# Performance work log

Measured on AMD Instinct MI355X. Metric: run time of the kernel, lower is better.

Reference implementation:

```python
import jax, jax.numpy as jnp
import numpy as np

B, LQ, LA, H = 32, 1024, 1024, 512
NEG_INF = jnp.float32(-1e7)  # matches torch masked_fill_(-10000000.0)


def setup_inputs() -> dict:
    key = jax.random.key(0)
    k1, k2, k3, k4 = jax.random.split(key, 4)
    q = jax.random.normal(k1, (B, LQ, H), dtype=jnp.float32)
    a = jax.random.normal(k2, (B, LA, H), dtype=jnp.float32)
    q_mask = jax.random.randint(k3, (B, LQ, 1), 0, 2).astype(jnp.int32)
    a_mask = jax.random.randint(k4, (B, LA, 1), 0, 2).astype(jnp.int32)
    # learned scalar, initialized exactly as in __init__
    temperature = jnp.float32(1.0 / np.sqrt(H))
    return {"q": q, "a": a, "q_mask": q_mask, "a_mask": a_mask,
            "temperature": temperature}


def reference(q, a, q_mask, a_mask, temperature):
    # scaled co-attention scores: [B, Lq, La]
    attn = jnp.einsum('bqh,bah->bqa', q, a) * temperature
    # validity mask via outer product of per-token masks (nonzero = valid)
    mask = jnp.matmul(q_mask.astype(jnp.float32),
                      a_mask.transpose(0, 2, 1).astype(jnp.float32)) != 0
    attn = jnp.where(mask, attn, NEG_INF)
    # dual-axis softmax over the SAME score matrix
    attn_q = jax.nn.softmax(attn, axis=1)  # normalize over Lq
    attn_a = jax.nn.softmax(attn, axis=2)  # normalize over La
    # aggregation: a_s = attn_q^T @ q -> [B, La, H]; q_s = attn_a @ a -> [B, Lq, H]
    a_s = jnp.einsum('bqa,bqh->bah', attn_q, q)
    q_s = jnp.einsum('bqa,bah->bqh', attn_a, a)
    return (jnp.concatenate([q, q_s], axis=-1),
            jnp.concatenate([a, a_s], axis=-1))
```

## Files before the change

### kernel.cpp

```cpp
#include <hip/hip_runtime.h>
#include <cstdint>
#include <cstddef>

#define NB   32
#define LQA  1024
#define HD   512

typedef __attribute__((ext_vector_type(4))) float  f32x4;
typedef __attribute__((ext_vector_type(8))) short  s16x8;
typedef __attribute__((ext_vector_type(4))) unsigned short u16x4;

static __device__ __forceinline__ unsigned short f2bf(float f) {
  unsigned int u = __builtin_bit_cast(unsigned int, f);
  u += 0x7fffu + ((u >> 16) & 1u);
  return (unsigned short)(u >> 16);
}
static __device__ __forceinline__ float bf2f(unsigned short h) {
  unsigned int u = ((unsigned int)h) << 16;
  return __builtin_bit_cast(float, u);
}
static __device__ __forceinline__ u16x4 cvt4(f32x4 v) {
  u16x4 r;
  r.x = f2bf(v.x); r.y = f2bf(v.y); r.z = f2bf(v.z); r.w = f2bf(v.w);
  return r;
}

typedef __attribute__((address_space(1))) const void gas_void;
typedef __attribute__((address_space(3))) void las_void;
static __device__ __forceinline__ void gload_lds16(const void* g, void* l) {
  __builtin_amdgcn_global_load_lds((gas_void*)g, (las_void*)l, 16, 0, 0);
}

__global__ __launch_bounds__(256) void k_prep(
    const float* __restrict__ qsrc, const float* __restrict__ asrc,
    float* __restrict__ out0, float* __restrict__ out1,
    unsigned short* __restrict__ qT, unsigned short* __restrict__ aT,
    unsigned short* __restrict__ qb16, unsigned short* __restrict__ ab16,
    float* __restrict__ qsum, float* __restrict__ asum)
{
  const int bz  = blockIdx.z;
  const int isA = bz >> 5;
  const int b   = bz & 31;
  const int h0 = blockIdx.x * 64;
  const int q0 = blockIdx.y * 64;
  const int t  = threadIdx.x;

  const float* src = isA ? asrc : qsrc;
  float* out_left      = isA ? out1 : out0;
  unsigned short* dstT = isA ? aT : qT;
  unsigned short* dstN = isA ? ab16 : qb16;
  float* csum          = isA ? asum : qsum;

  __shared__ unsigned short T[64 * 68];

  const float* sb = src + (size_t)b * LQA * HD;
  float* ob       = out_left + (size_t)b * LQA * 1024;
  unsigned short* db  = dstT + (size_t)b * HD * LQA;
  unsigned short* dbn = dstN + (size_t)b * LQA * HD;

#pragma unroll
  for (int j = 0; j < 4; ++j) {
    int f = t + 256 * j;
    int r = f >> 4;
    int c = (f & 15) * 4;
    f32x4 v = *(const f32x4*)(sb + (size_t)(q0 + r) * HD + h0 + c);
    *(f32x4*)(ob + (size_t)(q0 + r) * 1024 + h0 + c) = v;
    u16x4 cv = cvt4(v);
    *(u16x4*)&dbn[(size_t)(q0 + r) * HD + h0 + c] = cv;
    *(u16x4*)&T[r * 68 + c] = cv;
  }
  __syncthreads();
#pragma unroll
  for (int j = 0; j < 4; ++j) {
    int f = t + 256 * j;
    int orow = f >> 4;
    int c = (f & 15) * 4;
    u16x4 v;
    v.x = T[(c + 0) * 68 + orow];
    v.y = T[(c + 1) * 68 + orow];
    v.z = T[(c + 2) * 68 + orow];
    v.w = T[(c + 3) * 68 + orow];
    *(u16x4*)&db[(size_t)(h0 + orow) * LQA + q0 + c] = v;
    float s = bf2f(v.x) + bf2f(v.y) + bf2f(v.z) + bf2f(v.w);
    s += __shfl_xor(s, 1); s += __shfl_xor(s, 2);
    s += __shfl_xor(s, 4); s += __shfl_xor(s, 8);
    if ((t & 15) == 0)
      atomicAdd(&csum[(size_t)b * HD + h0 + orow], s);
  }
}

__global__ __launch_bounds__(256) void k_scores(
    const unsigned short* __restrict__ qb16, const unsigned short* __restrict__ ab16,
    const int* __restrict__ qmask, const int* __restrict__ amask,
    const float* __restrict__ temp_p,
    unsigned short* __restrict__ E, unsigned short* __restrict__ ET,
    float* __restrict__ rowsumE,
    float* __restrict__ colsumE)
{
  const int flat = blockIdx.x;
  const int xcd  = flat & 7;
  const int i5   = flat >> 3;
  const int b    = (i5 >> 6) * 8 + xcd;
  const int tile = i5 & 63;
  const int m0 = (tile & 7) * 128;
  const int n0 = (tile >> 3) * 128;

  const int t  = threadIdx.x;
  const int lane = t & 63;
  const int w  = t >> 6;
  const int moff = (w & 1) * 64;
  const int noff = (w >> 1) * 64;
  const int lrow = lane & 15;
  const int quad = lane >> 4;

  __shared__ __align__(16) unsigned short smem[128 * 132];
  unsigned short* As = smem;
  unsigned short* Bs = smem + 8192;

  const unsigned short* qb = qb16 + (size_t)b * LQA * HD;
  const unsigned short* ab = ab16 + (size_t)b * LQA * HD;

  const unsigned short* qg = qb + (size_t)(m0 + (t >> 3)) * HD + (t & 7) * 8;
  const unsigned short* ag = ab + (size_t)(n0 + (t >> 3)) * HD + (t & 7) * 8;

  f32x4 acc[4][4];
#pragma unroll
  for (int i = 0; i < 4; ++i)
#pragma unroll
    for (int j = 0; j < 4; ++j) acc[i][j] = (f32x4)0.f;

  for (int kt = 0; kt < HD / 64; ++kt) {
    const int ko = kt * 64;
#pragma unroll
    for (int p = 0; p < 4; ++p) {
      gload_lds16(qg + ko + p * 32 * HD, As + (w + 4 * p) * 512);
      gload_lds16(ag + ko + p * 32 * HD, Bs + (w + 4 * p) * 512);
    }
    __syncthreads();
#pragma unroll
    for (int ks = 0; ks < 2; ++ks) {
      s16x8 af[4], bfr[4];
#pragma unroll
      for (int i = 0; i < 4; ++i) {
        af[i]  = *(const s16x8*)&As[(moff + i * 16 + lrow) * 64 + ks * 32 + quad * 8];
        bfr[i] = *(const s16x8*)&Bs[(noff + i * 16 + lrow) * 64 + ks * 32 + quad * 8];
      }
#pragma unroll
      for (int i = 0; i < 4; ++i)
#pragma unroll
        for (int j = 0; j < 4; ++j)
          acc[i][j] = __builtin_amdgcn_mfma_f32_16x16x32_bf16(af[i], bfr[j], acc[i][j], 0, 0, 0);
    }
    __syncthreads();
  }

  unsigned short* Cs = smem;
  const float temp = temp_p[0];
  const int* qmb = qmask + b * LQA;
  const int* amb = amask + b * LQA;

  float rowp[4][4];
  float colp[4];
#pragma unroll
  for (int i = 0; i < 4; ++i)
#pragma unroll
    for (int r = 0; r < 4; ++r) rowp[i][r] = 0.f;
#pragma unroll
  for (int j = 0; j < 4; ++j) colp[j] = 0.f;

#pragma unroll
  for (int i = 0; i < 4; ++i) {
#pragma unroll
    for (int j = 0; j < 4; ++j) {
      int ncol = noff + j * 16 + lrow;
      float am = (amb[n0 + ncol] != 0) ? 1.f : 0.f;
#pragma unroll
      for (int r = 0; r < 4; ++r) {
        int mrow = moff + i * 16 + quad * 4 + r;
        float qm = (qmb[m0 + mrow] != 0) ? 1.f : 0.f;
        float e = __expf(acc[i][j][r] * temp) * am * qm;
        unsigned short eb = f2bf(e);
        float er = bf2f(eb);
        Cs[mrow * 132 + ncol] = eb;
        rowp[i][r] += er;
        colp[j] += er;
      }
    }
  }

#pragma unroll
  for (int i = 0; i < 4; ++i)
#pragma unroll
    for (int r = 0; r < 4; ++r) {
      float v = rowp[i][r];
      v += __shfl_xor(v, 1); v += __shfl_xor(v, 2);
      v += __shfl_xor(v, 4); v += __shfl_xor(v, 8);
      if (lrow == 0)
        atomicAdd(&rowsumE[(size_t)b * LQA + m0 + moff + i * 16 + quad * 4 + r], v);
    }
#pragma unroll
  for (int j = 0; j < 4; ++j) {
    float v = colp[j];
    v += __shfl_xor(v, 16); v += __shfl_xor(v, 32);
    if (quad == 0)
      atomicAdd(&colsumE[(size_t)b * LQA + n0 + noff + j * 16 + lrow], v);
  }

  __syncthreads();
  const size_t Ebase = (size_t)b * LQA * LQA;
#pragma unroll
  for (int jj = 0; jj < 16; ++jj) {
    int f = t + 256 * jj;
    int row = f >> 5;
    int c = (f & 31) * 4;
    u16x4 v = *(const u16x4*)&Cs[row * 132 + c];
    *(u16x4*)&E[Ebase + (size_t)(m0 + row) * LQA + n0 + c] = v;
  }
#pragma unroll
  for (int jj = 0; jj < 16; ++jj) {
    int f = t + 256 * jj;
    int orow = f >> 5;
    int c = (f & 31) * 4;
    u16x4 v;
    v.x = Cs[(c + 0) * 132 + orow];
    v.y = Cs[(c + 1) * 132 + orow];
    v.z = Cs[(c + 2) * 132 + orow];
    v.w = Cs[(c + 3) * 132 + orow];
    *(u16x4*)&ET[Ebase + (size_t)(n0 + orow) * LQA + m0 + c] = v;
  }
}

__global__ __launch_bounds__(256) void k_agg2(
    const unsigned short* __restrict__ Ein,
    const unsigned short* __restrict__ ETin,
    const unsigned short* __restrict__ qT,
    const unsigned short* __restrict__ aT,
    const float* __restrict__ sums,
    const float* __restrict__ qsum,
    const float* __restrict__ asum,
    float* __restrict__ out0, float* __restrict__ out1)
{
  const int flat  = blockIdx.x;
  const int half  = flat >> 10;
  const int inner = flat & 1023;
  const int xcd  = inner & 7;
  const int i5   = inner >> 3;
  const int b    = (i5 >> 5) * 8 + xcd;
  const int tile = i5 & 31;
  const int m0 = (tile & 7) * 128;
  const int n0 = (tile >> 3) * 128;

  const unsigned short* Emat = half ? ETin : Ein;
  const unsigned short* Bt   = half ? qT : aT;
  const float* srow = sums + (size_t)half * NB * LQA + (size_t)b * LQA;
  const float* bsp  = (half ? qsum : asum) + (size_t)b * HD;
  float* ob = (half ? out1 : out0) + (size_t)b * LQA * 1024;

  const int t  = threadIdx.x;
  const int lane = t & 63;
  const int w  = t >> 6;
  const int moff = (w & 1) * 64;
  const int noff = (w >> 1) * 64;
  const int lrow = lane & 15;
  const int quad = lane >> 4;

  __shared__ __align__(16) unsigned short As[128 * 64];
  __shared__ __align__(16) unsigned short Bs[128 * 64];

  const unsigned short* Eb = Emat + (size_t)b * LQA * LQA;
  const unsigned short* Bb = Bt + (size_t)b * HD * LQA;

  const unsigned short* eg = Eb + (size_t)(m0 + (t >> 3)) * LQA + (t & 7) * 8;
  const unsigned short* bg = Bb + (size_t)(n0 + (t >> 3)) * LQA + (t & 7) * 8;

  f32x4 acc[4][4];
#pragma unroll
  for (int i = 0; i < 4; ++i)
#pragma unroll
    for (int j = 0; j < 4; ++j) acc[i][j] = (f32x4)0.f;

  for (int kt = 0; kt < LQA / 64; ++kt) {
    const int ko = kt * 64;
#pragma unroll
    for (int p = 0; p < 4; ++p) {
      gload_lds16(eg + ko + p * 32 * LQA, As + (w + 4 * p) * 512);
      gload_lds16(bg + ko + p * 32 * LQA, Bs + (w + 4 * p) * 512);
    }
    __syncthreads();
#pragma unroll
    for (int ks = 0; ks < 2; ++ks) {
      s16x8 af[4], bfr[4];
#pragma unroll
      for (int i = 0; i < 4; ++i) {
        af[i]  = *(const s16x8*)&As[(moff + i * 16 + lrow) * 64 + ks * 32 + quad * 8];
        bfr[i] = *(const s16x8*)&Bs[(noff + i * 16 + lrow) * 64 + ks * 32 + quad * 8];
      }
#pragma unroll
      for (int i = 0; i < 4; ++i)
#pragma unroll
        for (int j = 0; j < 4; ++j)
          acc[i][j] = __builtin_amdgcn_mfma_f32_16x16x32_bf16(af[i], bfr[j], acc[i][j], 0, 0, 0);
    }
    __syncthreads();
  }

  float bcol[4];
#pragma unroll
  for (int j = 0; j < 4; ++j) bcol[j] = bsp[n0 + noff + j * 16 + lrow];
#pragma unroll
  for (int i = 0; i < 4; ++i) {
#pragma unroll
    for (int r = 0; r < 4; ++r) {
      int mrow = moff + i * 16 + quad * 4 + r;
      float s = srow[m0 + mrow];
      float inv = (s > 0.f) ? 1.f / s : 0.f;
      float add = (s > 0.f) ? 0.f : (1.f / 1024.f);
#pragma unroll
      for (int j = 0; j < 4; ++j) {
        int ncol = noff + j * 16 + lrow;
        ob[(size_t)(m0 + mrow) * 1024 + 512 + n0 + ncol] =
            inv * acc[i][j][r] + add * bcol[j];
      }
    }
  }
}

extern "C" void kernel_launch(void* const* d_in, const int* in_sizes, int n_in,
                              void* d_out, int out_size, void* d_ws, size_t ws_size,
                              hipStream_t stream) {
  (void)in_sizes; (void)n_in; (void)out_size; (void)ws_size;
  const float* q    = (const float*)d_in[0];
  const float* a    = (const float*)d_in[1];
  const int*   qm   = (const int*)d_in[2];
  const int*   am   = (const int*)d_in[3];
  const float* temp = (const float*)d_in[4];

  float* out0 = (float*)d_out;
  float* out1 = out0 + (size_t)NB * LQA * 1024;

  char* ws = (char*)d_ws;
  const size_t MB = 1024ull * 1024ull;
  unsigned short* E    = (unsigned short*)(ws);
  unsigned short* ET   = (unsigned short*)(ws + 64 * MB);
  unsigned short* qT   = (unsigned short*)(ws + 128 * MB);
  unsigned short* aT   = (unsigned short*)(ws + 160 * MB);
  unsigned short* qb16 = (unsigned short*)(ws + 192 * MB);
  unsigned short* ab16 = (unsigned short*)(ws + 224 * MB);
  float* sums = (float*)(ws + 256 * MB);
  float* qsum = (float*)(ws + 256 * MB + (256 << 10));
  float* asum = (float*)(ws + 256 * MB + (320 << 10));

  hipMemsetAsync(sums, 0, (size_t)(2 * NB * LQA + 2 * NB * HD) * sizeof(float), stream);
  k_prep<<<dim3(8, 16, 2 * NB), 256, 0, stream>>>(q, a, out0, out1, qT, aT,
                                                  qb16, ab16, qsum, asum);
  k_scores<<<dim3(2048), 256, 0, stream>>>(qb16, ab16, qm, am, temp,
                                           E, ET, sums, sums + NB * LQA);
  k_agg2<<<dim3(2048), 256, 0, stream>>>(E, ET, qT, aT, sums, qsum, asum,
                                         out0, out1);
}
```

Before: 616.7 us.

## Restructure aggregation GEMM into 128x512 tiles with triple-buffered async LDS pipeline

The aggregation kernel now computes a full 128-row by 512-column output tile per 512-thread block instead of 128x128 tiles, so each E row-block is read once rather than four times. The K loop uses 32-wide steps with a three-stage ring of LDS buffers filled by direct global-to-LDS loads, and explicit vmcnt waits let loads run ahead of the MFMA work. The block-to-batch mapping is also reordered across XCDs. In exchange the kernel uses more LDS and registers per block (32 accumulators per thread), which lowers occupancy, and the grid shrinks to 512 blocks.

Result: faster. 604.0 us (-2.1%).

```diff
diff --git a/kernel.cpp b/kernel.cpp
--- a/kernel.cpp
+++ b/kernel.cpp
@@ -230,7 +230,7 @@
   }
 }
 
-__global__ __launch_bounds__(256) void k_agg2(
+__global__ __launch_bounds__(512, 2) void k_agg2(
     const unsigned short* __restrict__ Ein,
     const unsigned short* __restrict__ ETin,
     const unsigned short* __restrict__ qT,
@@ -240,15 +240,12 @@
     const float* __restrict__ asum,
     float* __restrict__ out0, float* __restrict__ out1)
 {
-  const int flat  = blockIdx.x;
-  const int half  = flat >> 10;
-  const int inner = flat & 1023;
-  const int xcd  = inner & 7;
-  const int i5   = inner >> 3;
-  const int b    = (i5 >> 5) * 8 + xcd;
-  const int tile = i5 & 31;
-  const int m0 = (tile & 7) * 128;
-  const int n0 = (tile >> 3) * 128;
+  const int blk  = blockIdx.x;
+  const int L    = (blk & 7) * 64 + (blk >> 3);
+  const int half = L >> 8;
+  const int rem  = L & 255;
+  const int b    = rem >> 3;
+  const int m0   = (rem & 7) * 128;
 
   const unsigned short* Emat = half ? ETin : Ein;
   const unsigned short* Bt   = half ? qT : aT;
@@ -256,69 +253,92 @@
   const float* bsp  = (half ? qsum : asum) + (size_t)b * HD;
   float* ob = (half ? out1 : out0) + (size_t)b * LQA * 1024;
 
-  const int t  = threadIdx.x;
+  const int t    = threadIdx.x;
   const int lane = t & 63;
-  const int w  = t >> 6;
-  const int moff = (w & 1) * 64;
-  const int noff = (w >> 1) * 64;
+  const int w    = t >> 6;
+  const int wr   = w >> 2;
+  const int wc   = w & 3;
   const int lrow = lane & 15;
   const int quad = lane >> 4;
 
-  __shared__ __align__(16) unsigned short As[128 * 64];
-  __shared__ __align__(16) unsigned short Bs[128 * 64];
+  __shared__ __align__(16) unsigned short lds[3 * 20480];
 
   const unsigned short* Eb = Emat + (size_t)b * LQA * LQA;
   const unsigned short* Bb = Bt + (size_t)b * HD * LQA;
 
-  const unsigned short* eg = Eb + (size_t)(m0 + (t >> 3)) * LQA + (t & 7) * 8;
-  const unsigned short* bg = Bb + (size_t)(n0 + (t >> 3)) * LQA + (t & 7) * 8;
-
-  f32x4 acc[4][4];
+  const unsigned short* agp = Eb + (size_t)(m0 + (t >> 2)) * LQA + (t & 3) * 8;
+  const unsigned short* bgp[4];
+#pragma unroll
+  for (int p = 0; p < 4; ++p)
+    bgp[p] = Bb + (size_t)(128 * p + (t >> 2)) * LQA + (t & 3) * 8;
+  const int ldsA = w * 512;
+  const int ldsB = 4096 + w * 512;
+
+#define STAGE(kt, buf)                                                     \
+  do {                                                                     \
+    unsigned short* bp_ = lds + (buf) * 20480;                             \
+    const int ko_ = (kt) * 32;                                             \
+    gload_lds16(agp + ko_, bp_ + ldsA);                                    \
+    gload_lds16(bgp[0] + ko_, bp_ + ldsB);                                 \
+    gload_lds16(bgp[1] + ko_, bp_ + ldsB + 4096);                          \
+    gload_lds16(bgp[2] + ko_, bp_ + ldsB + 8192);                          \
+    gload_lds16(bgp[3] + ko_, bp_ + ldsB + 12288);                         \
+  } while (0)
+
+  f32x4 acc[4][8];
 #pragma unroll
   for (int i = 0; i < 4; ++i)
 #pragma unroll
-    for (int j = 0; j < 4; ++j) acc[i][j] = (f32x4)0.f;
-
-  for (int kt = 0; kt < LQA / 64; ++kt) {
-    const int ko = kt * 64;
-#pragma unroll
-    for (int p = 0; p < 4; ++p) {
-      gload_lds16(eg + ko + p * 32 * LQA, As + (w + 4 * p) * 512);
-      gload_lds16(bg + ko + p * 32 * LQA, Bs + (w + 4 * p) * 512);
-    }
-    __syncthreads();
-#pragma unroll
-    for (int ks = 0; ks < 2; ++ks) {
-      s16x8 af[4], bfr[4];
-#pragma unroll
-      for (int i = 0; i < 4; ++i) {
-        af[i]  = *(const s16x8*)&As[(moff + i * 16 + lrow) * 64 + ks * 32 + quad * 8];
-        bfr[i] = *(const s16x8*)&Bs[(noff + i * 16 + lrow) * 64 + ks * 32 + quad * 8];
-      }
-#pragma unroll
-      for (int i = 0; i < 4; ++i)
-#pragma unroll
-        for (int j = 0; j < 4; ++j)
-          acc[i][j] = __builtin_amdgcn_mfma_f32_16x16x32_bf16(af[i], bfr[j], acc[i][j], 0, 0, 0);
-    }
-    __syncthreads();
-  }
-
-  float bcol[4];
-#pragma unroll
-  for (int j = 0; j < 4; ++j) bcol[j] = bsp[n0 + noff + j * 16 + lrow];
+    for (int j = 0; j < 8; ++j) acc[i][j] = (f32x4)0.f;
+
+  STAGE(0, 0); STAGE(1, 1); STAGE(2, 2);
+
+  int cur = 0;
+  for (int k = 0; k < 32; ++k) {
+    if (k <= 29)      asm volatile("s_waitcnt vmcnt(10)");
+    else if (k == 30) asm volatile("s_waitcnt vmcnt(5)");
+    else              asm volatile("s_waitcnt vmcnt(0)");
+    __builtin_amdgcn_sched_barrier(0);
+    __builtin_amdgcn_s_barrier();
+    __builtin_amdgcn_sched_barrier(0);
+
+    const unsigned short* As = lds + cur * 20480;
+    const unsigned short* Bs = As + 4096;
+    s16x8 bfr[8];
+#pragma unroll
+    for (int j = 0; j < 8; ++j)
+      bfr[j] = *(const s16x8*)&Bs[(wc * 128 + j * 16 + lrow) * 32 + quad * 8];
+#pragma unroll
+    for (int i = 0; i < 4; ++i) {
+      s16x8 af = *(const s16x8*)&As[(wr * 64 + i * 16 + lrow) * 32 + quad * 8];
+#pragma unroll
+      for (int j = 0; j < 8; ++j)
+        acc[i][j] = __builtin_amdgcn_mfma_f32_16x16x32_bf16(af, bfr[j], acc[i][j], 0, 0, 0);
+    }
+
+    asm volatile("s_waitcnt lgkmcnt(0)");
+    __builtin_amdgcn_sched_barrier(0);
+    __builtin_amdgcn_s_barrier();
+    if (k + 3 < 32) STAGE(k + 3, cur);
+    cur = (cur == 2) ? 0 : cur + 1;
+  }
+#undef STAGE
+
+  float bcol[8];
+#pragma unroll
+  for (int j = 0; j < 8; ++j) bcol[j] = bsp[wc * 128 + j * 16 + lrow];
 #pragma unroll
   for (int i = 0; i < 4; ++i) {
 #pragma unroll
     for (int r = 0; r < 4; ++r) {
-      int mrow = moff + i * 16 + quad * 4 + r;
+      int mrow = wr * 64 + i * 16 + quad * 4 + r;
       float s = srow[m0 + mrow];
       float inv = (s > 0.f) ? 1.f / s : 0.f;
       float add = (s > 0.f) ? 0.f : (1.f / 1024.f);
 #pragma unroll
-      for (int j = 0; j < 4; ++j) {
-        int ncol = noff + j * 16 + lrow;
-        ob[(size_t)(m0 + mrow) * 1024 + 512 + n0 + ncol] =
+      for (int j = 0; j < 8; ++j) {
+        int ncol = wc * 128 + j * 16 + lrow;
+        ob[(size_t)(m0 + mrow) * 1024 + 512 + ncol] =
             inv * acc[i][j][r] + add * bcol[j];
       }
     }
@@ -355,6 +375,6 @@
                                                   qb16, ab16, qsum, asum);
   k_scores<<<dim3(2048), 256, 0, stream>>>(qb16, ab16, qm, am, temp,
                                            E, ET, sums, sums + NB * LQA);
-  k_agg2<<<dim3(2048), 256, 0, stream>>>(E, ET, qT, aT, sums, qsum, asum,
-                                         out0, out1);
-}
+  k_agg2<<<dim3(512), 512, 0, stream>>>(E, ET, qT, aT, sums, qsum, asum,
+                                        out0, out1);
+}
```
